# Kernel tuning notes

Measured on AMD Instinct MI355X. Metric: run time of the kernel, lower is better.

## Reference

```python
import jax, jax.numpy as jnp
import numpy as np

K, D, H, R, V = 4, 1024, 2048, 1024, 2048 + 4  # n_codebooks, d_model, hidden, repr, vocab
B, T = 4, 2048
LN_EPS = 1e-5


def setup_inputs() -> dict:
    key = jax.random.key(0)
    ks = jax.random.split(key, 9)
    s = 0.02
    return {
        "x": jax.random.normal(ks[0], (B, T, D), dtype=jnp.float32),
        "ln_scale": jnp.ones((K, D), dtype=jnp.float32),
        "ln_bias": jnp.zeros((K, D), dtype=jnp.float32),
        "W1": jax.random.normal(ks[1], (K, D, H), dtype=jnp.float32) * s,
        "b1": jnp.zeros((K, H), dtype=jnp.float32),
        "W2": jax.random.normal(ks[2], (K, H, R), dtype=jnp.float32) * s,
        "b2": jnp.zeros((K, R), dtype=jnp.float32),
        "Wc": jax.random.normal(ks[3], (K, R, V), dtype=jnp.float32) * s,
        "bc": jnp.zeros((K, V), dtype=jnp.float32),
    }


def reference(x, ln_scale, ln_bias, W1, b1, W2, b2, Wc, bc):
    # Shared x goes through each head's LayerNorm -> Linear -> GELU -> Linear -> classifier.
    # LayerNorm statistics depend only on x, so compute once and apply per-head affine.
    mu = jnp.mean(x, axis=-1, keepdims=True)
    var = jnp.mean(jnp.square(x - mu), axis=-1, keepdims=True)
    xn = (x - mu) * jax.lax.rsqrt(var + LN_EPS)              # [B,T,D]
    y = xn[:, None, :, :] * ln_scale[None, :, None, :] + ln_bias[None, :, None, :]  # [B,K,T,D]
    h = jax.nn.gelu(jnp.einsum('bktd,kdh->bkth', y, W1) + b1[None, :, None, :], approximate=False)
    g = jnp.einsum('bkth,khr->bktr', h, W2) + b2[None, :, None, :]   # repr [B,K,T,R]
    logits = jnp.einsum('bktr,krv->bktv', g, Wc) + bc[None, :, None, :]  # [B,K,T,V]
    return logits
```

## Files before the change

kernel.cpp:

```cpp
#include <hip/hip_runtime.h>
#include <cstdint>

#define KH   4
#define DM   1024
#define HID  2048
#define RP   1024
#define VOC  2052
#define VPAD 2304
#define TT   2048
#define MM   8192

typedef short bf16x8 __attribute__((ext_vector_type(8)));
typedef float f32x4  __attribute__((ext_vector_type(4)));

__device__ __forceinline__ unsigned short f2bf(float f) {
  union { float f; unsigned int u; } a; a.f = f;
  unsigned int u = a.u;
  unsigned int r = (u + 0x7fffu + ((u >> 16) & 1u)) >> 16;
  return (unsigned short)r;
}

__device__ __forceinline__ float fast_gelu(float v) {
  float u = v * (0.7978845608028654f + 0.035677408136300125f * v * v);
  float e = __expf(2.0f * u);
  float r = __builtin_amdgcn_rcpf(e + 1.0f);
  return v - v * r;
}

__device__ __forceinline__ void async_cp16(const unsigned short* g, unsigned short* l) {
  __builtin_amdgcn_global_load_lds(
      (const __attribute__((address_space(1))) unsigned int*)(uintptr_t)g,
      (__attribute__((address_space(3))) unsigned int*)(uintptr_t)l,
      16, 0, 0);
}

__global__ __launch_bounds__(256) void ln_kernel(const float* __restrict__ x,
                                                 unsigned short* __restrict__ xn) {
  int row = blockIdx.x;
  int tid = threadIdx.x;
  const float4* xr = (const float4*)(x + (size_t)row * DM);
  float4 v = xr[tid];
  float s  = v.x + v.y + v.z + v.w;
  float s2 = v.x * v.x + v.y * v.y + v.z * v.z + v.w * v.w;
  for (int o = 32; o > 0; o >>= 1) {
    s  += __shfl_down(s, o);
    s2 += __shfl_down(s2, o);
  }
  __shared__ float ps[8];
  int wave = tid >> 6, lane = tid & 63;
  if (lane == 0) { ps[wave] = s; ps[wave + 4] = s2; }
  __syncthreads();
  if (tid == 0) {
    float ts  = ps[0] + ps[1] + ps[2] + ps[3];
    float ts2 = ps[4] + ps[5] + ps[6] + ps[7];
    float mean = ts * (1.0f / DM);
    float var  = ts2 * (1.0f / DM) - mean * mean;
    ps[0] = mean;
    ps[1] = rsqrtf(var + 1e-5f);
  }
  __syncthreads();
  float mean = ps[0], rstd = ps[1];
  ushort4 o4;
  o4.x = f2bf((v.x - mean) * rstd);
  o4.y = f2bf((v.y - mean) * rstd);
  o4.z = f2bf((v.z - mean) * rstd);
  o4.w = f2bf((v.w - mean) * rstd);
  ((ushort4*)(xn + (size_t)row * DM))[tid] = o4;
}

__global__ __launch_bounds__(256) void fold_b1(const float* __restrict__ W1,
                                               const float* __restrict__ b1,
                                               const float* __restrict__ ln_bias,
                                               float* __restrict__ b1s) {
  int k  = blockIdx.y;
  int h0 = blockIdx.x * 64;
  int hl = threadIdx.x & 63;
  int dg = threadIdx.x >> 6;
  const float* Wk = W1 + (size_t)k * DM * HID;
  const float* lb = ln_bias + (size_t)k * DM;
  float acc = 0.f;
  for (int d = dg * 256; d < dg * 256 + 256; ++d)
    acc += lb[d] * Wk[(size_t)d * HID + h0 + hl];
  __shared__ float red[4][64];
  red[dg][hl] = acc;
  __syncthreads();
  if (dg == 0)
    b1s[(size_t)k * HID + h0 + hl] =
        b1[(size_t)k * HID + h0 + hl] + red[0][hl] + red[1][hl] + red[2][hl] + red[3][hl];
}

__global__ __launch_bounds__(256) void transpose_conv(const float* __restrict__ src,
                                                      unsigned short* __restrict__ dst,
                                                      const float* __restrict__ scale,
                                                      int Rr, int Cc, int Cpad,
                                                      int dstHeadStride) {
  int k  = blockIdx.z;
  int c0 = blockIdx.x * 32, r0 = blockIdx.y * 32;
  int tx = threadIdx.x & 31, ty = threadIdx.x >> 5;
  __shared__ float tile[32][33];
  const float* s = src + (size_t)k * Rr * Cc;
  for (int q = 0; q < 4; q++) {
    int r = r0 + ty + q * 8;
    int c = c0 + tx;
    float v = 0.f;
    if (c < Cc) v = s[(size_t)r * Cc + c];
    if (scale) v *= scale[(size_t)k * Rr + r];
    tile[ty + q * 8][tx] = v;
  }
  __syncthreads();
  unsigned short* d = dst + (size_t)k * dstHeadStride;
  for (int q = 0; q < 4; q++) {
    int c = c0 + ty + q * 8;
    int r = r0 + tx;
    if (c < Cpad) d[(size_t)c * Rr + r] = f2bf(tile[tx][ty + q * 8]);
  }
}


__device__ __forceinline__ void stage_half(const unsigned short* __restrict__ g, int ldK,
                                           unsigned short* l, int wave, int lane) {
#pragma unroll
  for (int r = 0; r < 2; ++r) {
    const int Pb  = r * 8192 + wave * 1024;
    const int P   = Pb + lane * 16;
    const int row = P >> 6;
    const int cb  = P & 63;
    async_cp16(g + (size_t)row * ldK + (cb >> 1), l + (Pb >> 1));
  }
}

#define LDSF(buf, off) (*(const bf16x8*)((buf) + (off)))

#define PH_PRE()                                      \
  __builtin_amdgcn_s_barrier();                       \
  asm volatile("s_waitcnt lgkmcnt(0)" ::: "memory"); \
  __builtin_amdgcn_s_setprio(1)

#define PH_POST() __builtin_amdgcn_s_setprio(0)

#define MROW(mi, a, B0, B1, B2, B3)                                                   \
  acc[mi][0] = __builtin_amdgcn_mfma_f32_16x16x32_bf16(a, B0, acc[mi][0], 0, 0, 0);   \
  acc[mi][1] = __builtin_amdgcn_mfma_f32_16x16x32_bf16(a, B1, acc[mi][1], 0, 0, 0);   \
  acc[mi][2] = __builtin_amdgcn_mfma_f32_16x16x32_bf16(a, B2, acc[mi][2], 0, 0, 0);   \
  acc[mi][3] = __builtin_amdgcn_mfma_f32_16x16x32_bf16(a, B3, acc[mi][3], 0, 0, 0);

#define TILE4(KT, CUR, NXT)                                                          \
  {                                                                                  \
    const bool st = ((KT) + 1) < nkt;                                                \
    const int kn = ((KT) + 1) << 6;                                                  \
    bf16x8 af0, af1, af2, af3, b00, b01, b02, b03, b10, b11, b12, b13;               \
                                                 \
    af0 = LDSF(As[CUR][0], aoff);                                                    \
    af1 = LDSF(As[CUR][0], aoff + 512);                                              \
    af2 = LDSF(As[CUR][0], aoff + 1024);                                             \
    af3 = LDSF(As[CUR][0], aoff + 1536);                                             \
    b00 = LDSF(Bs[CUR][0], boff);                                                    \
    b01 = LDSF(Bs[CUR][0], boff + 512);                                              \
    b02 = LDSF(Bs[CUR][0], boff + 1024);                                             \
    b03 = LDSF(Bs[CUR][0], boff + 1536);                                             \
    if (st) stage_half(gA + kn, Kd, &As[NXT][0][0], wave, lane);                     \
    PH_PRE();                                                                        \
    MROW(0, af0, b00, b01, b02, b03)                                                 \
    MROW(1, af1, b00, b01, b02, b03)                                                 \
    MROW(2, af2, b00, b01, b02, b03)                                                 \
    MROW(3, af3, b00, b01, b02, b03)                                                 \
    PH_POST();                                                                       \
    __builtin_amdgcn_s_barrier();                                                    \
                                                 \
    af0 = LDSF(As[CUR][0], aoff + 2048);                                             \
    af1 = LDSF(As[CUR][0], aoff + 2560);                                             \
    af2 = LDSF(As[CUR][0], aoff + 3072);                                             \
    af3 = LDSF(As[CUR][0], aoff + 3584);                                             \
    if (st) stage_half(gB + kn, Kd, &Bs[NXT][0][0], wave, lane);                     \
    PH_PRE();                                                                        \
    MROW(4, af0, b00, b01, b02, b03)                                                 \
    MROW(5, af1, b00, b01, b02, b03)                                                 \
    MROW(6, af2, b00, b01, b02, b03)                                                 \
    MROW(7, af3, b00, b01, b02, b03)                                                 \
    PH_POST();                                                                       \
    if (st) { asm volatile("s_waitcnt vmcnt(4)" ::: "memory"); }                     \
    else    { asm volatile("s_waitcnt vmcnt(0)" ::: "memory"); }                     \
    __builtin_amdgcn_s_barrier();                                                    \
                                                 \
    af0 = LDSF(As[CUR][1], aoff);                                                    \
    af1 = LDSF(As[CUR][1], aoff + 512);                                              \
    af2 = LDSF(As[CUR][1], aoff + 1024);                                             \
    af3 = LDSF(As[CUR][1], aoff + 1536);                                             \
    b10 = LDSF(Bs[CUR][1], boff);                                                    \
    b11 = LDSF(Bs[CUR][1], boff + 512);                                              \
    b12 = LDSF(Bs[CUR][1], boff + 1024);                                             \
    b13 = LDSF(Bs[CUR][1], boff + 1536);                                             \
    if (st) stage_half(gA + kn + 32, Kd, &As[NXT][1][0], wave, lane);                \
    PH_PRE();                                                                        \
    MROW(0, af0, b10, b11, b12, b13)                                                 \
    MROW(1, af1, b10, b11, b12, b13)                                                 \
    MROW(2, af2, b10, b11, b12, b13)                                                 \
    MROW(3, af3, b10, b11, b12, b13)                                                 \
    PH_POST();                                                                       \
    __builtin_amdgcn_s_barrier();                                                    \
                                                 \
    af0 = LDSF(As[CUR][1], aoff + 2048);                                             \
    af1 = LDSF(As[CUR][1], aoff + 2560);                                             \
    af2 = LDSF(As[CUR][1], aoff + 3072);                                             \
    af3 = LDSF(As[CUR][1], aoff + 3584);                                             \
    if (st) stage_half(gB + kn + 32, Kd, &Bs[NXT][1][0], wave, lane);                \
    PH_PRE();                                                                        \
    MROW(4, af0, b10, b11, b12, b13)                                                 \
    MROW(5, af1, b10, b11, b12, b13)                                                 \
    MROW(6, af2, b10, b11, b12, b13)                                                 \
    MROW(7, af3, b10, b11, b12, b13)                                                 \
    PH_POST();                                                                       \
    if (st) { asm volatile("s_waitcnt vmcnt(4)" ::: "memory"); }                     \
    __builtin_amdgcn_s_barrier();                                                    \
  }

template <int MODE>
__global__ __launch_bounds__(512, 2) void gemm_bt(const unsigned short* __restrict__ A,
                                                  size_t aStrideH,
                                                  const unsigned short* __restrict__ Bt,
                                                  size_t bStrideH,
                                                  const float* __restrict__ bias,
                                                  int biasStrideH,
                                                  unsigned short* __restrict__ ob,
                                                  size_t obStrideH,
                                                  float* __restrict__ of,
                                                  int Kd, int ldo, int khBase) {
  __shared__ __align__(16) unsigned short As[2][2][256 * 32];
  __shared__ __align__(16) unsigned short Bs[2][2][256 * 32];

  const int X = gridDim.x, Y = gridDim.y;
  const int lin = blockIdx.x + X * (blockIdx.y + Y * blockIdx.z);
  const int nwg = X * Y * gridDim.z;
  const int sw  = (lin & 7) * (nwg >> 3) + (lin >> 3);
  const int bx  = sw % X;
  const int t2  = sw / X;
  const int by  = t2 % Y;
  const int kh  = t2 / Y + khBase;

  A    += (size_t)kh * aStrideH;
  Bt   += (size_t)kh * bStrideH;
  bias += (size_t)kh * biasStrideH;
  ob   += (size_t)kh * obStrideH;

  const int tile_m = by * 256;
  const int tile_n = bx * 256;
  const int tid  = threadIdx.x;
  const int wave = tid >> 6;
  const int lane = tid & 63;
  const int wr = wave >> 2;
  const int wc = wave & 3;
  const int al = lane & 15;
  const int kq = lane >> 4;
  const int aoff = (wr * 128 + al) * 32 + kq * 8;
  const int boff = (wc * 64 + al) * 32 + kq * 8;

  const unsigned short* gA = A  + (size_t)tile_m * Kd;
  const unsigned short* gB = Bt + (size_t)tile_n * Kd;
  const int nkt = Kd >> 6;

  f32x4 acc[8][4];
#pragma unroll
  for (int i = 0; i < 8; i++)
#pragma unroll
    for (int j = 0; j < 4; j++) acc[i][j] = (f32x4){0.f, 0.f, 0.f, 0.f};

  stage_half(gA,      Kd, &As[0][0][0], wave, lane);
  stage_half(gB,      Kd, &Bs[0][0][0], wave, lane);
  stage_half(gA + 32, Kd, &As[0][1][0], wave, lane);
  stage_half(gB + 32, Kd, &Bs[0][1][0], wave, lane);
  asm volatile("s_waitcnt vmcnt(4)" ::: "memory");
  __builtin_amdgcn_s_barrier();

#pragma unroll 1
  for (int kt = 0; kt < nkt; kt += 2) {
    TILE4(kt, 0, 1);
    TILE4(kt + 1, 1, 0);
  }

  const int rg = kq * 4;
#pragma unroll
  for (int nj = 0; nj < 4; ++nj) {
    const int gcol = tile_n + wc * 64 + nj * 16 + al;
    float bj = 0.f;
    if (MODE != 2 || gcol < VOC) bj = bias[gcol];
#pragma unroll
    for (int mi = 0; mi < 8; ++mi) {
      const int grow = tile_m + wr * 128 + mi * 16 + rg;
#pragma unroll
      for (int r = 0; r < 4; ++r) {
        float v = acc[mi][nj][r] + bj;
        if (MODE == 0) {
          ob[(size_t)(grow + r) * ldo + gcol] = f2bf(fast_gelu(v));
        } else if (MODE == 1) {
          ob[(size_t)(grow + r) * ldo + gcol] = f2bf(v);
        } else {
          if (gcol < VOC) {
            int m = grow + r;
            int b = m >> 11, t = m & 2047;
            of[((size_t)(b * KH + kh) * TT + t) * VOC + gcol] = v;
          }
        }
      }
    }
  }
}

extern "C" void kernel_launch(void* const* d_in, const int* in_sizes, int n_in,
                              void* d_out, int out_size, void* d_ws, size_t ws_size,
                              hipStream_t stream) {
  const float* x        = (const float*)d_in[0];
  const float* ln_scale = (const float*)d_in[1];
  const float* ln_bias  = (const float*)d_in[2];
  const float* W1       = (const float*)d_in[3];
  const float* b1       = (const float*)d_in[4];
  const float* W2       = (const float*)d_in[5];
  const float* b2       = (const float*)d_in[6];
  const float* Wc       = (const float*)d_in[7];
  const float* bc       = (const float*)d_in[8];
  float* out = (float*)d_out;

  char* p = (char*)d_ws;
  auto alloc = [&](size_t bytes) {
    char* r = p;
    p += (bytes + 255) & ~(size_t)255;
    return r;
  };
  unsigned short* xn  = (unsigned short*)alloc((size_t)MM * DM * 2);
  unsigned short* w1t = (unsigned short*)alloc((size_t)KH * HID * DM * 2);
  float*          b1s = (float*)alloc((size_t)KH * HID * 4);
  unsigned short* w2t = (unsigned short*)alloc((size_t)KH * RP * HID * 2);
  unsigned short* wct = (unsigned short*)alloc((size_t)KH * VPAD * RP * 2);

  const size_t fixed = (size_t)(p - (char*)d_ws);
  const size_t needBatched = fixed + ((size_t)KH * MM * HID * 2 + 256) + ((size_t)KH * MM * RP * 2 + 256);
  const bool batched = ws_size >= needBatched;

  unsigned short* hbuf;
  unsigned short* gbuf;
  size_t hStride, gStride;
  if (batched) {
    hbuf = (unsigned short*)alloc((size_t)KH * MM * HID * 2);
    gbuf = (unsigned short*)alloc((size_t)KH * MM * RP * 2);
    hStride = (size_t)MM * HID;
    gStride = (size_t)MM * RP;
  } else {
    hbuf = (unsigned short*)alloc((size_t)MM * HID * 2);
    gbuf = (unsigned short*)alloc((size_t)MM * RP * 2);
    hStride = 0;
    gStride = 0;
  }

  ln_kernel<<<MM, 256, 0, stream>>>(x, xn);
  fold_b1<<<dim3(HID / 64, KH), 256, 0, stream>>>(W1, b1, ln_bias, b1s);
  transpose_conv<<<dim3(HID / 32, DM / 32, KH), 256, 0, stream>>>(W1, w1t, ln_scale, DM, HID, HID, HID * DM);
  transpose_conv<<<dim3(RP / 32, HID / 32, KH), 256, 0, stream>>>(W2, w2t, nullptr, HID, RP, RP, RP * HID);
  transpose_conv<<<dim3(VPAD / 32, RP / 32, KH), 256, 0, stream>>>(Wc, wct, nullptr, RP, VOC, VPAD, VPAD * RP);

  if (batched) {
    gemm_bt<0><<<dim3(HID / 256, MM / 256, KH), 512, 0, stream>>>(
        xn, 0, w1t, (size_t)HID * DM, b1s, HID, hbuf, hStride, nullptr, DM, HID, 0);
    gemm_bt<1><<<dim3(RP / 256, MM / 256, KH), 512, 0, stream>>>(
        hbuf, hStride, w2t, (size_t)RP * HID, b2, RP, gbuf, gStride, nullptr, HID, RP, 0);
    gemm_bt<2><<<dim3(VPAD / 256, MM / 256, KH), 512, 0, stream>>>(
        gbuf, gStride, wct, (size_t)VPAD * RP, bc, VOC, nullptr, 0, out, RP, 0, 0);
  } else {
    for (int kh = 0; kh < KH; kh++) {
      gemm_bt<0><<<dim3(HID / 256, MM / 256, 1), 512, 0, stream>>>(
          xn, 0, w1t + (size_t)kh * HID * DM, 0, b1s + (size_t)kh * HID, 0,
          hbuf, 0, nullptr, DM, HID, kh);
      gemm_bt<1><<<dim3(RP / 256, MM / 256, 1), 512, 0, stream>>>(
          hbuf, 0, w2t + (size_t)kh * RP * HID, 0, b2 + (size_t)kh * RP, 0,
          gbuf, 0, nullptr, HID, RP, kh);
      gemm_bt<2><<<dim3(VPAD / 256, MM / 256, 1), 512, 0, stream>>>(
          gbuf, 0, wct + (size_t)kh * VPAD * RP, 0, bc + (size_t)kh * VOC, 0,
          nullptr, 0, out, RP, 0, kh);
    }
  }
}
```

Before: 950.7 us.

## Split bias-fold reduction across D and reorder LDS tile layout for MFMA reads

```diff
diff --git a/kernel.cpp b/kernel.cpp
--- a/kernel.cpp
+++ b/kernel.cpp
@@ -68,25 +68,36 @@
   ((ushort4*)(xn + (size_t)row * DM))[tid] = o4;
 }
 
-__global__ __launch_bounds__(256) void fold_b1(const float* __restrict__ W1,
-                                               const float* __restrict__ b1,
-                                               const float* __restrict__ ln_bias,
-                                               float* __restrict__ b1s) {
+__global__ __launch_bounds__(256) void fold_b1_part(const float* __restrict__ W1,
+                                                    const float* __restrict__ ln_bias,
+                                                    float* __restrict__ part) {
   int k  = blockIdx.y;
+  int z  = blockIdx.z;
   int h0 = blockIdx.x * 64;
   int hl = threadIdx.x & 63;
   int dg = threadIdx.x >> 6;
   const float* Wk = W1 + (size_t)k * DM * HID;
   const float* lb = ln_bias + (size_t)k * DM;
   float acc = 0.f;
-  for (int d = dg * 256; d < dg * 256 + 256; ++d)
+  int d0 = z * 128 + dg * 32;
+  for (int d = d0; d < d0 + 32; ++d)
     acc += lb[d] * Wk[(size_t)d * HID + h0 + hl];
   __shared__ float red[4][64];
   red[dg][hl] = acc;
   __syncthreads();
   if (dg == 0)
-    b1s[(size_t)k * HID + h0 + hl] =
-        b1[(size_t)k * HID + h0 + hl] + red[0][hl] + red[1][hl] + red[2][hl] + red[3][hl];
+    part[((size_t)z * KH + k) * HID + h0 + hl] =
+        red[0][hl] + red[1][hl] + red[2][hl] + red[3][hl];
+}
+
+__global__ __launch_bounds__(256) void fold_b1_fin(const float* __restrict__ part,
+                                                   const float* __restrict__ b1,
+                                                   float* __restrict__ b1s) {
+  int i = blockIdx.x * 256 + threadIdx.x;
+  float s = b1[i];
+#pragma unroll
+  for (int z = 0; z < 8; ++z) s += part[(size_t)z * KH * HID + i];
+  b1s[i] = s;
 }
 
 __global__ __launch_bounds__(256) void transpose_conv(const float* __restrict__ src,
@@ -121,11 +132,9 @@
                                            unsigned short* l, int wave, int lane) {
 #pragma unroll
   for (int r = 0; r < 2; ++r) {
-    const int Pb  = r * 8192 + wave * 1024;
-    const int P   = Pb + lane * 16;
-    const int row = P >> 6;
-    const int cb  = P & 63;
-    async_cp16(g + (size_t)row * ldK + (cb >> 1), l + (Pb >> 1));
+    const int b = wave * 2 + r;
+    async_cp16(g + (size_t)(b * 16 + (lane & 15)) * ldK + (lane >> 4) * 8,
+               l + b * 512);
   }
 }
 
@@ -251,8 +260,8 @@
   const int wc = wave & 3;
   const int al = lane & 15;
   const int kq = lane >> 4;
-  const int aoff = (wr * 128 + al) * 32 + kq * 8;
-  const int boff = (wc * 64 + al) * 32 + kq * 8;
+  const int aoff = wr * 4096 + kq * 128 + al * 8;
+  const int boff = wc * 2048 + kq * 128 + al * 8;
 
   const unsigned short* gA = A  + (size_t)tile_m * Kd;
   const unsigned short* gB = Bt + (size_t)tile_n * Kd;
@@ -325,11 +334,12 @@
     p += (bytes + 255) & ~(size_t)255;
     return r;
   };
-  unsigned short* xn  = (unsigned short*)alloc((size_t)MM * DM * 2);
-  unsigned short* w1t = (unsigned short*)alloc((size_t)KH * HID * DM * 2);
-  float*          b1s = (float*)alloc((size_t)KH * HID * 4);
-  unsigned short* w2t = (unsigned short*)alloc((size_t)KH * RP * HID * 2);
-  unsigned short* wct = (unsigned short*)alloc((size_t)KH * VPAD * RP * 2);
+  unsigned short* xn   = (unsigned short*)alloc((size_t)MM * DM * 2);
+  unsigned short* w1t  = (unsigned short*)alloc((size_t)KH * HID * DM * 2);
+  float*          b1s  = (float*)alloc((size_t)KH * HID * 4);
+  float*          b1p  = (float*)alloc((size_t)8 * KH * HID * 4);
+  unsigned short* w2t  = (unsigned short*)alloc((size_t)KH * RP * HID * 2);
+  unsigned short* wct  = (unsigned short*)alloc((size_t)KH * VPAD * RP * 2);
 
   const size_t fixed = (size_t)(p - (char*)d_ws);
   const size_t needBatched = fixed + ((size_t)KH * MM * HID * 2 + 256) + ((size_t)KH * MM * RP * 2 + 256);
@@ -351,7 +361,8 @@
   }
 
   ln_kernel<<<MM, 256, 0, stream>>>(x, xn);
-  fold_b1<<<dim3(HID / 64, KH), 256, 0, stream>>>(W1, b1, ln_bias, b1s);
+  fold_b1_part<<<dim3(HID / 64, KH, 8), 256, 0, stream>>>(W1, ln_bias, b1p);
+  fold_b1_fin<<<dim3(KH * HID / 256), 256, 0, stream>>>(b1p, b1, b1s);
   transpose_conv<<<dim3(HID / 32, DM / 32, KH), 256, 0, stream>>>(W1, w1t, ln_scale, DM, HID, HID, HID * DM);
   transpose_conv<<<dim3(RP / 32, HID / 32, KH), 256, 0, stream>>>(W2, w2t, nullptr, HID, RP, RP, RP * HID);
   transpose_conv<<<dim3(VPAD / 32, RP / 32, KH), 256, 0, stream>>>(Wc, wct, nullptr, RP, VOC, VPAD, VPAD * RP);
```

Result: slower. 975.2 us (+2.6%).
